# Kernel optimization log

Measured on AMD Instinct MI355X. Metric: run time of the kernel, lower is better.

## Reference

```python
import jax, jax.numpy as jnp
import numpy as np

T, N, E = 6, 50000, 1600000
NFEAT, NHID, NCLASS = 256, 256, 16
SLOPE = 11.0 / 48.0  # eval-mode RReLU: mean of default (lower=1/8, upper=1/3)


def _grcu(H_seq, src, dst, val, Wz, Uz, bz, Wr, Ur, br, Wh, Uh, bh, Q0):
    """One GRCU layer: matrix-GRU weight evolution + sparse GCN aggregation per step.
    H_seq: [T, N, in]  src/dst: [T, E] int  val: [T, E]  Q0: [in, out]."""
    n = H_seq.shape[1]

    def step(Q, xs):
        H, s, d, v = xs
        # mat_GRU_cell: x = hidden = prev_Q (z_topk path is unused in this repo's forward)
        z = jax.nn.sigmoid(Wz @ Q + Uz @ Q + bz)
        r = jax.nn.sigmoid(Wr @ Q + Ur @ Q + br)
        h = jnp.tanh(Wh @ Q + Uh @ (r * Q) + bh)
        Qn = (1.0 - z) * Q + z * h
        XW = H @ Qn                                   # [N, out]
        msg = v[:, None] * XW[s]                      # per-edge gather: Ahat row weights
        agg = jax.ops.segment_sum(msg, d, num_segments=n)  # Ahat @ (H @ Qn)
        out = jnp.where(agg >= 0, agg, SLOPE * agg)   # RReLU (eval)
        return Qn, out

    _, out_seq = jax.lax.scan(step, Q0, (H_seq, src, dst, val))
    return out_seq  # [T, N, out]


def setup_inputs() -> dict:
    key = jax.random.key(0)
    ks = iter(jax.random.split(key, 64))

    def rn(shape, scale=0.05):
        return jax.random.normal(next(ks), shape, dtype=jnp.float32) * scale

    inp = {
        "node_feats": jax.random.normal(next(ks), (T, N, NFEAT), dtype=jnp.float32),
        "edge_val": jax.random.uniform(next(ks), (T, E), dtype=jnp.float32),
    }
    for l, (fi, fo) in enumerate([(NFEAT, NHID), (NHID, NHID)]):
        for g in ("z", "r", "h"):
            inp[f"l{l}_W{g}"] = rn((fi, fi))
            inp[f"l{l}_U{g}"] = rn((fi, fi))
            inp[f"l{l}_b{g}"] = jnp.zeros((fi, fo), dtype=jnp.float32)
        inp[f"l{l}_Q0"] = rn((fi, fo))
    inp["mlp_W1"] = rn((NHID, NHID))
    inp["mlp_b1"] = jnp.zeros((NHID,), dtype=jnp.float32)
    inp["mlp_W2"] = rn((NHID, NCLASS))
    inp["mlp_b2"] = jnp.zeros((NCLASS,), dtype=jnp.float32)
    inp["edge_src"] = jax.random.randint(next(ks), (T, E), 0, N, dtype=jnp.int32)
    inp["edge_dst"] = jax.random.randint(next(ks), (T, E), 0, N, dtype=jnp.int32)
    return inp


def reference(node_feats, edge_val,
              l0_Wz, l0_Uz, l0_bz, l0_Wr, l0_Ur, l0_br, l0_Wh, l0_Uh, l0_bh, l0_Q0,
              l1_Wz, l1_Uz, l1_bz, l1_Wr, l1_Ur, l1_br, l1_Wh, l1_Uh, l1_bh, l1_Q0,
              mlp_W1, mlp_b1, mlp_W2, mlp_b2,
              edge_src, edge_dst):
    h1 = _grcu(node_feats, edge_src, edge_dst, edge_val,
               l0_Wz, l0_Uz, l0_bz, l0_Wr, l0_Ur, l0_br, l0_Wh, l0_Uh, l0_bh, l0_Q0)
    h2 = _grcu(h1, edge_src, edge_dst, edge_val,
               l1_Wz, l1_Uz, l1_bz, l1_Wr, l1_Ur, l1_br, l1_Wh, l1_Uh, l1_bh, l1_Q0)
    out = h2[-1]                                    # last timestep, [N, nhid]
    hid = jax.nn.relu(out @ mlp_W1 + mlp_b1)
    logits = hid @ mlp_W2 + mlp_b2
    return jax.nn.log_softmax(logits, axis=1)       # [N, nclass]
```

## Files before the change

### kernel.cpp

```cpp
#include <hip/hip_runtime.h>
#include <cstddef>

#define SLOPE_F (11.0f / 48.0f)

static const int NN = 50000;
static const int EE = 1600000;
static const int D  = 256;

typedef __attribute__((ext_vector_type(8))) short short8;
typedef __attribute__((ext_vector_type(4))) float f32x4;

__device__ __forceinline__ ushort f2bf(float f) {
    unsigned u = __float_as_uint(f);
    unsigned r = (u + 0x7fffu + ((u >> 16) & 1u)) >> 16;
    return (ushort)r;
}
__device__ __forceinline__ float bf2f(ushort u) {
    return __uint_as_float(((unsigned)u) << 16);
}

__global__ __launch_bounds__(256) void prep_kernel(
        const float* __restrict__ Wz0, const float* __restrict__ Uz0,
        const float* __restrict__ Wr0, const float* __restrict__ Ur0,
        const float* __restrict__ Wh0, const float* __restrict__ Uh0,
        const float* __restrict__ Wz1, const float* __restrict__ Uz1,
        const float* __restrict__ Wr1, const float* __restrict__ Ur1,
        const float* __restrict__ Wh1, const float* __restrict__ Uh1,
        const float* __restrict__ W1,
        float* __restrict__ TW, ushort* __restrict__ BtW1, int* __restrict__ deg) {
    int b = blockIdx.x;
    int t = threadIdx.x;
    if (b < 2048) {
        int mat = b >> 8;
        int k = b & 255;
        const float* P = nullptr; const float* S = nullptr;
        switch (mat) {
            case 0: P = Wz0; S = Uz0; break;
            case 1: P = Wr0; S = Ur0; break;
            case 2: P = Wh0; break;
            case 3: P = Uh0; break;
            case 4: P = Wz1; S = Uz1; break;
            case 5: P = Wr1; S = Ur1; break;
            case 6: P = Wh1; break;
            default: P = Uh1; break;
        }
        float v = P[t * 256 + k];
        if (S) v += S[t * 256 + k];
        TW[((size_t)mat * 256 + k) * 256 + t] = v;
    } else if (b < 2304) {
        int n = b - 2048;
        BtW1[(size_t)n * 256 + t] = f2bf(W1[t * 256 + n]);
    } else {
        int i = (b - 2304) * 256 + t;
        if (i < NN) deg[i] = 0;
    }
}

__global__ __launch_bounds__(256) void gruhist_kernel(
        const float* __restrict__ TW,
        const float* __restrict__ bz0, const float* __restrict__ br0,
        const float* __restrict__ bh0, const float* __restrict__ Q00,
        const float* __restrict__ bz1, const float* __restrict__ br1,
        const float* __restrict__ bh1, const float* __restrict__ Q01,
        ushort* __restrict__ Bt,
        const int* __restrict__ dst, int* __restrict__ deg) {
    if (blockIdx.x >= 256) {
        int e = (blockIdx.x - 256) * 256 + threadIdx.x;
        if (e < EE) atomicAdd(&deg[dst[e]], 1);
        return;
    }
    __shared__ float qs[256][2];
    __shared__ float rqs[256][2];
    int layer = blockIdx.x >> 7;
    int j0 = (blockIdx.x & 127) * 2;
    int i = threadIdx.x;
    const float* MzT = TW + (size_t)layer * 4 * 65536;
    const float* MrT = MzT + 65536;
    const float* WhT = MzT + 2 * 65536;
    const float* UhT = MzT + 3 * 65536;
    const float* bz = layer ? bz1 : bz0;
    const float* br = layer ? br1 : br0;
    const float* bh = layer ? bh1 : bh0;
    const float* Q0 = layer ? Q01 : Q00;

    float2 bzv = *(const float2*)&bz[i * 256 + j0];
    float2 brv = *(const float2*)&br[i * 256 + j0];
    float2 bhv = *(const float2*)&bh[i * 256 + j0];
    float bza[2] = {bzv.x, bzv.y};
    float bra[2] = {brv.x, brv.y};
    float bha[2] = {bhv.x, bhv.y};

    float2 qv = *(const float2*)&Q0[i * 256 + j0];
    *(float2*)&qs[i][0] = qv;
    __syncthreads();

    float qn[2] = {qv.x, qv.y};
    for (int step = 0; step < 6; ++step) {
        float az[2] = {}, ar[2] = {}, ah[2] = {};
#pragma unroll 8
        for (int k = 0; k < 256; ++k) {
            float mz = MzT[k * 256 + i];
            float mr = MrT[k * 256 + i];
            float wh = WhT[k * 256 + i];
            float2 qk = *(const float2*)&qs[k][0];
            float qa[2] = {qk.x, qk.y};
#pragma unroll
            for (int c = 0; c < 2; ++c) {
                az[c] += mz * qa[c];
                ar[c] += mr * qa[c];
                ah[c] += wh * qa[c];
            }
        }
        float z[2], qo[2];
        float2 qown = *(const float2*)&qs[i][0];
        qo[0] = qown.x; qo[1] = qown.y;
        float rq[2];
#pragma unroll
        for (int c = 0; c < 2; ++c) {
            z[c] = 1.f / (1.f + expf(-(az[c] + bza[c])));
            float r = 1.f / (1.f + expf(-(ar[c] + bra[c])));
            rq[c] = r * qo[c];
        }
        float2 rqv; rqv.x = rq[0]; rqv.y = rq[1];
        *(float2*)&rqs[i][0] = rqv;
        __syncthreads();
        float bu[2] = {};
#pragma unroll 8
        for (int k = 0; k < 256; ++k) {
            float uh = UhT[k * 256 + i];
            float2 rk = *(const float2*)&rqs[k][0];
#pragma unroll
            for (int c = 0; c < 2; ++c) bu[c] += uh * ((c == 0) ? rk.x : rk.y);
        }
        float2 qnv;
#pragma unroll
        for (int c = 0; c < 2; ++c) {
            float h = tanhf(ah[c] + bu[c] + bha[c]);
            qn[c] = (1.f - z[c]) * qo[c] + z[c] * h;
        }
        qnv.x = qn[0]; qnv.y = qn[1];
        *(float2*)&qs[i][0] = qnv;
        __syncthreads();
    }
#pragma unroll
    for (int c = 0; c < 2; ++c)
        Bt[(size_t)layer * 65536 + (size_t)(j0 + c) * 256 + i] = f2bf(qn[c]);
}

template <int ASRC, int EPI>
__global__ __launch_bounds__(256) void gemm_mfma(const ushort* __restrict__ A,
                                                 const float* __restrict__ Af,
                                                 const ushort* __restrict__ Bt,
                                                 const float* __restrict__ bias,
                                                 ushort* __restrict__ C, int M) {
    int tid = threadIdx.x;
    int w = tid >> 6, l = tid & 63;
    int lr = l & 15;
    int lk = l >> 4;
    int row0 = blockIdx.x * 128 + w * 32;
    int ra = row0 + lr;      if (ra > M - 1) ra = M - 1;
    int rb = row0 + 16 + lr; if (rb > M - 1) rb = M - 1;
    const ushort* Ap0  = A  + (size_t)ra * 256 + lk * 8;
    const ushort* Ap1  = A  + (size_t)rb * 256 + lk * 8;
    const float*  Apf0 = Af + (size_t)ra * 256 + lk * 8;
    const float*  Apf1 = Af + (size_t)rb * 256 + lk * 8;
    const ushort* Bp   = Bt + (size_t)lr * 256 + lk * 8;

    f32x4 acc0[16] = {};
    f32x4 acc1[16] = {};
#pragma unroll
    for (int kc = 0; kc < 8; ++kc) {
        short8 a0, a1;
        if (ASRC == 0) {
            a0 = *(const short8*)(Ap0 + kc * 32);
            a1 = *(const short8*)(Ap1 + kc * 32);
        } else {
            float4 f0 = *(const float4*)(Apf0 + kc * 32);
            float4 f1 = *(const float4*)(Apf0 + kc * 32 + 4);
            float4 g0 = *(const float4*)(Apf1 + kc * 32);
            float4 g1 = *(const float4*)(Apf1 + kc * 32 + 4);
            a0[0] = (short)f2bf(f0.x); a0[1] = (short)f2bf(f0.y);
            a0[2] = (short)f2bf(f0.z); a0[3] = (short)f2bf(f0.w);
            a0[4] = (short)f2bf(f1.x); a0[5] = (short)f2bf(f1.y);
            a0[6] = (short)f2bf(f1.z); a0[7] = (short)f2bf(f1.w);
            a1[0] = (short)f2bf(g0.x); a1[1] = (short)f2bf(g0.y);
            a1[2] = (short)f2bf(g0.z); a1[3] = (short)f2bf(g0.w);
            a1[4] = (short)f2bf(g1.x); a1[5] = (short)f2bf(g1.y);
            a1[6] = (short)f2bf(g1.z); a1[7] = (short)f2bf(g1.w);
        }
#pragma unroll
        for (int nb = 0; nb < 16; ++nb) {
            short8 bf = *(const short8*)(Bp + (size_t)nb * 4096 + kc * 32);
            acc0[nb] = __builtin_amdgcn_mfma_f32_16x16x32_bf16(a0, bf, acc0[nb], 0, 0, 0);
            acc1[nb] = __builtin_amdgcn_mfma_f32_16x16x32_bf16(a1, bf, acc1[nb], 0, 0, 0);
        }
    }

    int ro = lk * 4;
#pragma unroll
    for (int nb = 0; nb < 16; ++nb) {
        int gc = nb * 16 + lr;
        float bb = (EPI == 1) ? bias[gc] : 0.f;
#pragma unroll
        for (int q = 0; q < 4; ++q) {
            int g0 = row0 + ro + q;
            if (g0 < M) {
                float v = acc0[nb][q];
                if (EPI == 1) v = fmaxf(v + bb, 0.f);
                C[(size_t)g0 * 256 + gc] = f2bf(v);
            }
            int g1 = row0 + 16 + ro + q;
            if (g1 < M) {
                float v = acc1[nb][q];
                if (EPI == 1) v = fmaxf(v + bb, 0.f);
                C[(size_t)g1 * 256 + gc] = f2bf(v);
            }
        }
    }
}

__global__ __launch_bounds__(256) void scanA_kernel(const int* __restrict__ deg,
                                                    int* __restrict__ rs,
                                                    int* __restrict__ bsum, int n) {
    __shared__ int wsum[4];
    int tid = threadIdx.x;
    int i = blockIdx.x * 256 + tid;
    int lane = tid & 63, wv = tid >> 6;
    int v = (i < n) ? deg[i] : 0;
    int x = v;
#pragma unroll
    for (int off = 1; off < 64; off <<= 1) {
        int t = __shfl_up(x, off, 64);
        if (lane >= off) x += t;
    }
    if (lane == 63) wsum[wv] = x;
    __syncthreads();
    if (tid == 0) {
        int s = 0;
#pragma unroll
        for (int q = 0; q < 4; ++q) { int t = wsum[q]; wsum[q] = s; s += t; }
        bsum[blockIdx.x] = s;
    }
    __syncthreads();
    if (i < n) rs[i] = wsum[wv] + x - v;
}

__global__ __launch_bounds__(256) void scanB_kernel(const int* __restrict__ bsum,
                                                    int* __restrict__ boff,
                                                    int* __restrict__ rs, int nb) {
    __shared__ int wsum[4];
    int tid = threadIdx.x;
    int lane = tid & 63, wv = tid >> 6;
    int v = (tid < nb) ? bsum[tid] : 0;
    int x = v;
#pragma unroll
    for (int off = 1; off < 64; off <<= 1) {
        int t = __shfl_up(x, off, 64);
        if (lane >= off) x += t;
    }
    if (lane == 63) wsum[wv] = x;
    __syncthreads();
    if (tid == 0) {
        int s = 0;
#pragma unroll
        for (int q = 0; q < 4; ++q) { int t = wsum[q]; wsum[q] = s; s += t; }
        rs[NN] = EE;
    }
    __syncthreads();
    if (tid < nb) boff[tid] = wsum[wv] + x - v;
}

__global__ __launch_bounds__(256) void scanC_kernel(int* __restrict__ rs,
                                                    int* __restrict__ cur,
                                                    const int* __restrict__ boff, int n) {
    int i = blockIdx.x * 256 + threadIdx.x;
    if (i < n) {
        int v = rs[i] + boff[blockIdx.x];
        rs[i] = v;
        cur[i] = v;
    }
}

__global__ void scatter_kernel(const int* __restrict__ src, const int* __restrict__ dst,
                               const float* __restrict__ val, int* __restrict__ cur,
                               unsigned long long* __restrict__ csr, int nE) {
    int e = blockIdx.x * blockDim.x + threadIdx.x;
    if (e < nE) {
        int p = atomicAdd(&cur[dst[e]], 1);
        unsigned long long pk = (unsigned long long)(unsigned)src[e]
                              | ((unsigned long long)(unsigned)__float_as_uint(val[e]) << 32);
        __builtin_nontemporal_store(pk, &csr[p]);
    }
}

__global__ __launch_bounds__(256) void agg_csr_kernel(const ushort* __restrict__ XW,
                                                      const int2* __restrict__ csr,
                                                      const int* __restrict__ rs,
                                                      ushort* __restrict__ out) {
    int d = blockIdx.x * 4 + (threadIdx.x >> 6);
    if (d >= NN) return;
    int l = threadIdx.x & 63;
    int h = l >> 5;
    int il = l & 31;
    int beg = rs[d], end = rs[d + 1];
    float a0 = 0.f, a1 = 0.f, a2 = 0.f, a3 = 0.f;
    float a4 = 0.f, a5 = 0.f, a6 = 0.f, a7 = 0.f;
    int i = beg + h;
    for (; i + 14 < end; i += 16) {
        int2 e[8];
        short8 x[8];
#pragma unroll
        for (int u = 0; u < 8; ++u) e[u] = csr[i + 2 * u];
#pragma unroll
        for (int u = 0; u < 8; ++u)
            x[u] = *(const short8*)&XW[(size_t)e[u].x * D + il * 8];
#pragma unroll
        for (int u = 0; u < 8; ++u) {
            float v = __int_as_float(e[u].y);
            a0 += v * bf2f((ushort)x[u][0]);
            a1 += v * bf2f((ushort)x[u][1]);
            a2 += v * bf2f((ushort)x[u][2]);
            a3 += v * bf2f((ushort)x[u][3]);
            a4 += v * bf2f((ushort)x[u][4]);
            a5 += v * bf2f((ushort)x[u][5]);
            a6 += v * bf2f((ushort)x[u][6]);
            a7 += v * bf2f((ushort)x[u][7]);
        }
    }
    for (; i + 6 < end; i += 8) {
        int2 e[4];
        short8 x[4];
#pragma unroll
        for (int u = 0; u < 4; ++u) e[u] = csr[i + 2 * u];
#pragma unroll
        for (int u = 0; u < 4; ++u)
            x[u] = *(const short8*)&XW[(size_t)e[u].x * D + il * 8];
#pragma unroll
        for (int u = 0; u < 4; ++u) {
            float v = __int_as_float(e[u].y);
            a0 += v * bf2f((ushort)x[u][0]);
            a1 += v * bf2f((ushort)x[u][1]);
            a2 += v * bf2f((ushort)x[u][2]);
            a3 += v * bf2f((ushort)x[u][3]);
            a4 += v * bf2f((ushort)x[u][4]);
            a5 += v * bf2f((ushort)x[u][5]);
            a6 += v * bf2f((ushort)x[u][6]);
            a7 += v * bf2f((ushort)x[u][7]);
        }
    }
    for (; i < end; i += 2) {
        int2 e0 = csr[i];
        float v0 = __int_as_float(e0.y);
        short8 x0 = *(const short8*)&XW[(size_t)e0.x * D + il * 8];
        a0 += v0 * bf2f((ushort)x0[0]); a1 += v0 * bf2f((ushort)x0[1]);
        a2 += v0 * bf2f((ushort)x0[2]); a3 += v0 * bf2f((ushort)x0[3]);
        a4 += v0 * bf2f((ushort)x0[4]); a5 += v0 * bf2f((ushort)x0[5]);
        a6 += v0 * bf2f((ushort)x0[6]); a7 += v0 * bf2f((ushort)x0[7]);
    }
    a0 += __shfl_xor(a0, 32); a1 += __shfl_xor(a1, 32);
    a2 += __shfl_xor(a2, 32); a3 += __shfl_xor(a3, 32);
    a4 += __shfl_xor(a4, 32); a5 += __shfl_xor(a5, 32);
    a6 += __shfl_xor(a6, 32); a7 += __shfl_xor(a7, 32);
    if (h == 0) {
        float r[8] = {a0, a1, a2, a3, a4, a5, a6, a7};
        short8 o;
#pragma unroll
        for (int c = 0; c < 8; ++c) {
            float v = r[c];
            v = (v >= 0.f) ? v : SLOPE_F * v;
            o[c] = (short)f2bf(v);
        }
        *(short8*)&out[(size_t)d * D + il * 8] = o;
    }
}

__global__ void mlp2_kernel(const ushort* __restrict__ hid, const float* __restrict__ W2,
                            const float* __restrict__ b2, float* __restrict__ out, int M) {
    int tid = threadIdx.x;
    int n = blockIdx.x * 16 + (tid >> 4);
    int c = tid & 15;
    if (n >= M) return;
    float acc = b2[c];
    const ushort* hp = hid + (size_t)n * D;
    for (int k = 0; k < D; k += 8) {
        short8 h8 = *(const short8*)(hp + k);
#pragma unroll
        for (int u = 0; u < 8; ++u)
            acc += bf2f((ushort)h8[u]) * W2[(k + u) * 16 + c];
    }
    float m = acc;
#pragma unroll
    for (int off = 1; off < 16; off <<= 1)
        m = fmaxf(m, __shfl_xor(m, off, 16));
    float ex = expf(acc - m);
    float s = ex;
#pragma unroll
    for (int off = 1; off < 16; off <<= 1)
        s += __shfl_xor(s, off, 16);
    out[(size_t)n * 16 + c] = acc - m - logf(s);
}

extern "C" void kernel_launch(void* const* d_in, const int* in_sizes, int n_in,
                              void* d_out, int out_size, void* d_ws, size_t ws_size,
                              hipStream_t stream) {
    const float* node_feats = (const float*)d_in[0];
    const float* edge_val   = (const float*)d_in[1];
    const float* l0_Wz = (const float*)d_in[2];
    const float* l0_Uz = (const float*)d_in[3];
    const float* l0_bz = (const float*)d_in[4];
    const float* l0_Wr = (const float*)d_in[5];
    const float* l0_Ur = (const float*)d_in[6];
    const float* l0_br = (const float*)d_in[7];
    const float* l0_Wh = (const float*)d_in[8];
    const float* l0_Uh = (const float*)d_in[9];
    const float* l0_bh = (const float*)d_in[10];
    const float* l0_Q0 = (const float*)d_in[11];
    const float* l1_Wz = (const float*)d_in[12];
    const float* l1_Uz = (const float*)d_in[13];
    const float* l1_bz = (const float*)d_in[14];
    const float* l1_Wr = (const float*)d_in[15];
    const float* l1_Ur = (const float*)d_in[16];
    const float* l1_br = (const float*)d_in[17];
    const float* l1_Wh = (const float*)d_in[18];
    const float* l1_Uh = (const float*)d_in[19];
    const float* l1_bh = (const float*)d_in[20];
    const float* l1_Q0 = (const float*)d_in[21];
    const float* W1 = (const float*)d_in[22];
    const float* b1 = (const float*)d_in[23];
    const float* W2 = (const float*)d_in[24];
    const float* b2 = (const float*)d_in[25];
    const int* e_src = (const int*)d_in[26];
    const int* e_dst = (const int*)d_in[27];
    float* out = (float*)d_out;

    const size_t BIG = (size_t)NN * D;
    ushort* XWb = (ushort*)d_ws;
    ushort* H   = XWb + BIG;
    ushort* Bt  = H + BIG;
    float*  TW  = (float*)(Bt + 3 * 65536);
    int2*   csr = (int2*)(TW + 8 * 65536);
    int*    deg = (int*)(csr + EE);
    int*    rs  = deg + NN;
    int*    cur = rs + NN + 1;
    int*    bsum = cur + NN;
    int*    boff = bsum + 200;

    const float* feats5 = node_feats + (size_t)5 * BIG;
    const int*   src5   = e_src + (size_t)5 * EE;
    const int*   dst5   = e_dst + (size_t)5 * EE;
    const float* val5   = edge_val + (size_t)5 * EE;

    prep_kernel<<<2500, 256, 0, stream>>>(l0_Wz, l0_Uz, l0_Wr, l0_Ur, l0_Wh, l0_Uh,
                                          l1_Wz, l1_Uz, l1_Wr, l1_Ur, l1_Wh, l1_Uh,
                                          W1, TW, Bt + 2 * 65536, deg);

    const int histblocks = (EE + 255) / 256;
    gruhist_kernel<<<256 + histblocks, 256, 0, stream>>>(TW, l0_bz, l0_br, l0_bh, l0_Q0,
                                                         l1_bz, l1_br, l1_bh, l1_Q0, Bt,
                                                         dst5, deg);

    const int nchunks = (NN + 255) / 256;
    scanA_kernel<<<nchunks, 256, 0, stream>>>(deg, rs, bsum, NN);
    scanB_kernel<<<1, 256, 0, stream>>>(bsum, boff, rs, nchunks);
    scanC_kernel<<<nchunks, 256, 0, stream>>>(rs, cur, boff, NN);
    scatter_kernel<<<(EE + 255) / 256, 256, 0, stream>>>(src5, dst5, val5, cur,
                                                         (unsigned long long*)csr, EE);

    const int gemm_blocks = (NN + 127) / 128;
    const int ablocks = (NN + 3) / 4;

    gemm_mfma<1, 0><<<gemm_blocks, 256, 0, stream>>>(nullptr, feats5, Bt + 0 * 65536,
                                                     nullptr, XWb, NN);
    agg_csr_kernel<<<ablocks, 256, 0, stream>>>(XWb, csr, rs, H);

    gemm_mfma<0, 0><<<gemm_blocks, 256, 0, stream>>>(H, nullptr, Bt + 1 * 65536,
                                                     nullptr, XWb, NN);
    agg_csr_kernel<<<ablocks, 256, 0, stream>>>(XWb, csr, rs, H);

    gemm_mfma<0, 1><<<gemm_blocks, 256, 0, stream>>>(H, nullptr, Bt + 2 * 65536,
                                                     b1, XWb, NN);
    mlp2_kernel<<<(NN + 15) / 16, 256, 0, stream>>>(XWb, W2, b2, out, NN);
}
```

Before: 685.9 us.

## Merge preprocessing, scan and scatter stages into fewer fused kernel launches

```diff
diff --git a/kernel.cpp b/kernel.cpp
--- a/kernel.cpp
+++ b/kernel.cpp
@@ -6,6 +6,8 @@
 static const int NN = 50000;
 static const int EE = 1600000;
 static const int D  = 256;
+static const int NCH = 196;
+static const int GB  = 391;
 
 typedef __attribute__((ext_vector_type(8))) short short8;
 typedef __attribute__((ext_vector_type(4))) float f32x4;
@@ -19,7 +21,7 @@
     return __uint_as_float(((unsigned)u) << 16);
 }
 
-__global__ __launch_bounds__(256) void prep_kernel(
+__global__ __launch_bounds__(256) void prephist_kernel(
         const float* __restrict__ Wz0, const float* __restrict__ Uz0,
         const float* __restrict__ Wr0, const float* __restrict__ Ur0,
         const float* __restrict__ Wh0, const float* __restrict__ Uh0,
@@ -27,12 +29,19 @@
         const float* __restrict__ Wr1, const float* __restrict__ Ur1,
         const float* __restrict__ Wh1, const float* __restrict__ Uh1,
         const float* __restrict__ W1,
-        float* __restrict__ TW, ushort* __restrict__ BtW1, int* __restrict__ deg) {
+        float* __restrict__ TW, ushort* __restrict__ BtW1,
+        const int* __restrict__ dst, int* __restrict__ deg) {
     int b = blockIdx.x;
-    int t = threadIdx.x;
-    if (b < 2048) {
-        int mat = b >> 8;
-        int k = b & 255;
+    int tid = threadIdx.x;
+    if (b >= 144) {
+        int e = (b - 144) * 256 + tid;
+        if (e < EE) atomicAdd(&deg[dst[e]], 1);
+        return;
+    }
+    __shared__ float lt[64][65];
+    if (b < 128) {
+        int mat = b >> 4;
+        int tr = (b >> 2) & 3, tc = b & 3;
         const float* P = nullptr; const float* S = nullptr;
         switch (mat) {
             case 0: P = Wz0; S = Uz0; break;
@@ -44,36 +53,104 @@
             case 6: P = Wh1; break;
             default: P = Uh1; break;
         }
-        float v = P[t * 256 + k];
-        if (S) v += S[t * 256 + k];
-        TW[((size_t)mat * 256 + k) * 256 + t] = v;
-    } else if (b < 2304) {
-        int n = b - 2048;
-        BtW1[(size_t)n * 256 + t] = f2bf(W1[t * 256 + n]);
+#pragma unroll
+        for (int r0 = 0; r0 < 64; r0 += 4) {
+            int r = r0 + (tid >> 6);
+            int c = tid & 63;
+            int row = tr * 64 + r, col = tc * 64 + c;
+            float v = P[row * 256 + col];
+            if (S) v += S[row * 256 + col];
+            lt[r][c] = v;
+        }
+        __syncthreads();
+#pragma unroll
+        for (int c0 = 0; c0 < 64; c0 += 4) {
+            int c = c0 + (tid >> 6);
+            int r = tid & 63;
+            int row = tr * 64 + r, col = tc * 64 + c;
+            TW[((size_t)mat * 256 + col) * 256 + row] = lt[r][c];
+        }
     } else {
-        int i = (b - 2304) * 256 + t;
-        if (i < NN) deg[i] = 0;
-    }
-}
-
-__global__ __launch_bounds__(256) void gruhist_kernel(
+        int t = b - 128;
+        int tr = (t >> 2) & 3, tc = t & 3;
+#pragma unroll
+        for (int r0 = 0; r0 < 64; r0 += 4) {
+            int r = r0 + (tid >> 6);
+            int c = tid & 63;
+            lt[r][c] = W1[(tr * 64 + r) * 256 + tc * 64 + c];
+        }
+        __syncthreads();
+#pragma unroll
+        for (int c0 = 0; c0 < 64; c0 += 4) {
+            int c = c0 + (tid >> 6);
+            int r = tid & 63;
+            BtW1[(size_t)(tc * 64 + c) * 256 + tr * 64 + r] = f2bf(lt[r][c]);
+        }
+    }
+}
+
+__global__ __launch_bounds__(256) void gruscan_kernel(
         const float* __restrict__ TW,
         const float* __restrict__ bz0, const float* __restrict__ br0,
         const float* __restrict__ bh0, const float* __restrict__ Q00,
         const float* __restrict__ bz1, const float* __restrict__ br1,
         const float* __restrict__ bh1, const float* __restrict__ Q01,
         ushort* __restrict__ Bt,
-        const int* __restrict__ dst, int* __restrict__ deg) {
-    if (blockIdx.x >= 256) {
-        int e = (blockIdx.x - 256) * 256 + threadIdx.x;
-        if (e < EE) atomicAdd(&deg[dst[e]], 1);
+        const int* __restrict__ deg, int* __restrict__ rs, int* __restrict__ cur,
+        int* __restrict__ bsum, int* __restrict__ boff, int* __restrict__ done) {
+    int tid = threadIdx.x;
+    if (blockIdx.x >= 128) {
+        __shared__ int wsum[4];
+        __shared__ int lastflag;
+        int blk = blockIdx.x - 128;
+        int i = blk * 256 + tid;
+        int lane = tid & 63, wv = tid >> 6;
+        int v = (i < NN) ? deg[i] : 0;
+        int x = v;
+#pragma unroll
+        for (int off = 1; off < 64; off <<= 1) {
+            int t = __shfl_up(x, off, 64);
+            if (lane >= off) x += t;
+        }
+        if (lane == 63) wsum[wv] = x;
+        __syncthreads();
+        if (tid == 0) {
+            int s = 0;
+#pragma unroll
+            for (int q = 0; q < 4; ++q) { int t = wsum[q]; wsum[q] = s; s += t; }
+            bsum[blk] = s;
+        }
+        __syncthreads();
+        if (i < NN) { int p = wsum[wv] + x - v; rs[i] = p; cur[i] = p; }
+        __threadfence();
+        if (tid == 0) lastflag = (atomicAdd(done, 1) == NCH - 1);
+        __syncthreads();
+        if (lastflag) {
+            __threadfence();
+            int bv = (tid < NCH) ? bsum[tid] : 0;
+            int bx = bv;
+#pragma unroll
+            for (int off = 1; off < 64; off <<= 1) {
+                int t = __shfl_up(bx, off, 64);
+                if (lane >= off) bx += t;
+            }
+            if (lane == 63) wsum[wv] = bx;
+            __syncthreads();
+            if (tid == 0) {
+                int s = 0;
+#pragma unroll
+                for (int q = 0; q < 4; ++q) { int t = wsum[q]; wsum[q] = s; s += t; }
+            }
+            __syncthreads();
+            if (tid < NCH) boff[tid] = wsum[wv] + bx - bv;
+        }
         return;
     }
-    __shared__ float qs[256][2];
-    __shared__ float rqs[256][2];
-    int layer = blockIdx.x >> 7;
-    int j0 = (blockIdx.x & 127) * 2;
-    int i = threadIdx.x;
+    __shared__ float qs[256][4];
+    __shared__ float rqs[256][4];
+    int layer = blockIdx.x >> 6;
+    int j0 = (blockIdx.x & 63) * 4;
+    int i = tid;
     const float* MzT = TW + (size_t)layer * 4 * 65536;
     const float* MrT = MzT + 65536;
     const float* WhT = MzT + 2 * 65536;
@@ -83,81 +160,82 @@
     const float* bh = layer ? bh1 : bh0;
     const float* Q0 = layer ? Q01 : Q00;
 
-    float2 bzv = *(const float2*)&bz[i * 256 + j0];
-    float2 brv = *(const float2*)&br[i * 256 + j0];
-    float2 bhv = *(const float2*)&bh[i * 256 + j0];
-    float bza[2] = {bzv.x, bzv.y};
-    float bra[2] = {brv.x, brv.y};
-    float bha[2] = {bhv.x, bhv.y};
-
-    float2 qv = *(const float2*)&Q0[i * 256 + j0];
-    *(float2*)&qs[i][0] = qv;
+    float4 bzv = *(const float4*)&bz[i * 256 + j0];
+    float4 brv = *(const float4*)&br[i * 256 + j0];
+    float4 bhv = *(const float4*)&bh[i * 256 + j0];
+    float bza[4] = {bzv.x, bzv.y, bzv.z, bzv.w};
+    float bra[4] = {brv.x, brv.y, brv.z, brv.w};
+    float bha[4] = {bhv.x, bhv.y, bhv.z, bhv.w};
+
+    float4 qv = *(const float4*)&Q0[i * 256 + j0];
+    *(float4*)&qs[i][0] = qv;
     __syncthreads();
 
-    float qn[2] = {qv.x, qv.y};
+    float qn[4] = {qv.x, qv.y, qv.z, qv.w};
     for (int step = 0; step < 6; ++step) {
-        float az[2] = {}, ar[2] = {}, ah[2] = {};
-#pragma unroll 8
+        float az[4] = {}, ar[4] = {}, ah[4] = {};
+#pragma unroll 4
         for (int k = 0; k < 256; ++k) {
             float mz = MzT[k * 256 + i];
             float mr = MrT[k * 256 + i];
             float wh = WhT[k * 256 + i];
-            float2 qk = *(const float2*)&qs[k][0];
-            float qa[2] = {qk.x, qk.y};
-#pragma unroll
-            for (int c = 0; c < 2; ++c) {
+            float4 qk = *(const float4*)&qs[k][0];
+            float qa[4] = {qk.x, qk.y, qk.z, qk.w};
+#pragma unroll
+            for (int c = 0; c < 4; ++c) {
                 az[c] += mz * qa[c];
                 ar[c] += mr * qa[c];
                 ah[c] += wh * qa[c];
             }
         }
-        float z[2], qo[2];
-        float2 qown = *(const float2*)&qs[i][0];
-        qo[0] = qown.x; qo[1] = qown.y;
-        float rq[2];
-#pragma unroll
-        for (int c = 0; c < 2; ++c) {
+        float z[4], qo[4];
+        float4 qown = *(const float4*)&qs[i][0];
+        qo[0] = qown.x; qo[1] = qown.y; qo[2] = qown.z; qo[3] = qown.w;
+        float rq[4];
+#pragma unroll
+        for (int c = 0; c < 4; ++c) {
             z[c] = 1.f / (1.f + expf(-(az[c] + bza[c])));
             float r = 1.f / (1.f + expf(-(ar[c] + bra[c])));
             rq[c] = r * qo[c];
         }
-        float2 rqv; rqv.x = rq[0]; rqv.y = rq[1];
-        *(float2*)&rqs[i][0] = rqv;
-        __syncthreads();
-        float bu[2] = {};
-#pragma unroll 8
+        float4 rqv; rqv.x = rq[0]; rqv.y = rq[1]; rqv.z = rq[2]; rqv.w = rq[3];
+        *(float4*)&rqs[i][0] = rqv;
+        __syncthreads();
+        float bu[4] = {};
+#pragma unroll 4
         for (int k = 0; k < 256; ++k) {
             float uh = UhT[k * 256 + i];
-            float2 rk = *(const float2*)&rqs[k][0];
-#pragma unroll
-            for (int c = 0; c < 2; ++c) bu[c] += uh * ((c == 0) ? rk.x : rk.y);
-        }
-        float2 qnv;
-#pragma unroll
-        for (int c = 0; c < 2; ++c) {
+            float4 rk = *(const float4*)&rqs[k][0];
+            float ra[4] = {rk.x, rk.y, rk.z, rk.w};
+#pragma unroll
+            for (int c = 0; c < 4; ++c) bu[c] += uh * ra[c];
+        }
+        float4 qnv;
+#pragma unroll
+        for (int c = 0; c < 4; ++c) {
             float h = tanhf(ah[c] + bu[c] + bha[c]);
             qn[c] = (1.f - z[c]) * qo[c] + z[c] * h;
         }
-        qnv.x = qn[0]; qnv.y = qn[1];
-        *(float2*)&qs[i][0] = qnv;
-        __syncthreads();
-    }
-#pragma unroll
-    for (int c = 0; c < 2; ++c)
+        qnv.x = qn[0]; qnv.y = qn[1]; qnv.z = qn[2]; qnv.w = qn[3];
+        *(float4*)&qs[i][0] = qnv;
+        __syncthreads();
+    }
+#pragma unroll
+    for (int c = 0; c < 4; ++c)
         Bt[(size_t)layer * 65536 + (size_t)(j0 + c) * 256 + i] = f2bf(qn[c]);
 }
 
 template <int ASRC, int EPI>
-__global__ __launch_bounds__(256) void gemm_mfma(const ushort* __restrict__ A,
-                                                 const float* __restrict__ Af,
-                                                 const ushort* __restrict__ Bt,
-                                                 const float* __restrict__ bias,
-                                                 ushort* __restrict__ C, int M) {
-    int tid = threadIdx.x;
+__device__ __forceinline__ void gemm_body(int bid, int tid,
+                                          const ushort* __restrict__ A,
+                                          const float* __restrict__ Af,
+                                          const ushort* __restrict__ Bt,
+                                          const float* __restrict__ bias,
+                                          ushort* __restrict__ C, int M) {
     int w = tid >> 6, l = tid & 63;
     int lr = l & 15;
     int lk = l >> 4;
-    int row0 = blockIdx.x * 128 + w * 32;
+    int row0 = bid * 128 + w * 32;
     int ra = row0 + lr;      if (ra > M - 1) ra = M - 1;
     int rb = row0 + 16 + lr; if (rb > M - 1) rb = M - 1;
     const ushort* Ap0  = A  + (size_t)ra * 256 + lk * 8;
@@ -219,74 +297,32 @@
     }
 }
 
-__global__ __launch_bounds__(256) void scanA_kernel(const int* __restrict__ deg,
-                                                    int* __restrict__ rs,
-                                                    int* __restrict__ bsum, int n) {
-    __shared__ int wsum[4];
-    int tid = threadIdx.x;
-    int i = blockIdx.x * 256 + tid;
-    int lane = tid & 63, wv = tid >> 6;
-    int v = (i < n) ? deg[i] : 0;
-    int x = v;
-#pragma unroll
-    for (int off = 1; off < 64; off <<= 1) {
-        int t = __shfl_up(x, off, 64);
-        if (lane >= off) x += t;
-    }
-    if (lane == 63) wsum[wv] = x;
-    __syncthreads();
-    if (tid == 0) {
-        int s = 0;
-#pragma unroll
-        for (int q = 0; q < 4; ++q) { int t = wsum[q]; wsum[q] = s; s += t; }
-        bsum[blockIdx.x] = s;
-    }
-    __syncthreads();
-    if (i < n) rs[i] = wsum[wv] + x - v;
-}
-
-__global__ __launch_bounds__(256) void scanB_kernel(const int* __restrict__ bsum,
-                                                    int* __restrict__ boff,
-                                                    int* __restrict__ rs, int nb) {
-    __shared__ int wsum[4];
-    int tid = threadIdx.x;
-    int lane = tid & 63, wv = tid >> 6;
-    int v = (tid < nb) ? bsum[tid] : 0;
-    int x = v;
-#pragma unroll
-    for (int off = 1; off < 64; off <<= 1) {
-        int t = __shfl_up(x, off, 64);
-        if (lane >= off) x += t;
-    }
-    if (lane == 63) wsum[wv] = x;
-    __syncthreads();
-    if (tid == 0) {
-        int s = 0;
-#pragma unroll
-        for (int q = 0; q < 4; ++q) { int t = wsum[q]; wsum[q] = s; s += t; }
-        rs[NN] = EE;
-    }
-    __syncthreads();
-    if (tid < nb) boff[tid] = wsum[wv] + x - v;
-}
-
-__global__ __launch_bounds__(256) void scanC_kernel(int* __restrict__ rs,
-                                                    int* __restrict__ cur,
-                                                    const int* __restrict__ boff, int n) {
-    int i = blockIdx.x * 256 + threadIdx.x;
-    if (i < n) {
-        int v = rs[i] + boff[blockIdx.x];
-        rs[i] = v;
-        cur[i] = v;
-    }
-}
-
-__global__ void scatter_kernel(const int* __restrict__ src, const int* __restrict__ dst,
-                               const float* __restrict__ val, int* __restrict__ cur,
-                               unsigned long long* __restrict__ csr, int nE) {
-    int e = blockIdx.x * blockDim.x + threadIdx.x;
-    if (e < nE) {
-        int p = atomicAdd(&cur[dst[e]], 1);
+template <int ASRC, int EPI>
+__global__ __launch_bounds__(256) void gemm_mfma(const ushort* __restrict__ A,
+                                                 const float* __restrict__ Af,
+                                                 const ushort* __restrict__ Bt,
+                                                 const float* __restrict__ bias,
+                                                 ushort* __restrict__ C, int M) {
+    gemm_body<ASRC, EPI>(blockIdx.x, threadIdx.x, A, Af, Bt, bias, C, M);
+}
+
+__global__ __launch_bounds__(256) void gemsca_kernel(const float* __restrict__ Af,
+                                                     const ushort* __restrict__ Bt,
+                                                     ushort* __restrict__ C, int M,
+                                                     const int* __restrict__ src,
+                                                     const int* __restrict__ dst,
+                                                     const float* __restrict__ val,
+                                                     int* __restrict__ cur,
+                                                     const int* __restrict__ boff,
+                                                     unsigned long long* __restrict__ csr) {
+    if (blockIdx.x < GB) {
+        gemm_body<1, 0>(blockIdx.x, threadIdx.x, nullptr, Af, Bt, nullptr, C, M);
+        return;
+    }
+    int e = (blockIdx.x - GB) * 256 + threadIdx.x;
+    if (e < EE) {
+        int d = dst[e];
+        int p = atomicAdd(&cur[d], 1) + boff[d >> 8];
         unsigned long long pk = (unsigned long long)(unsigned)src[e]
                               | ((unsigned long long)(unsigned)__float_as_uint(val[e]) << 32);
         __builtin_nontemporal_store(pk, &csr[p]);
@@ -296,13 +332,15 @@
 __global__ __launch_bounds__(256) void agg_csr_kernel(const ushort* __restrict__ XW,
                                                       const int2* __restrict__ csr,
                                                       const int* __restrict__ rs,
+                                                      const int* __restrict__ boff,
                                                       ushort* __restrict__ out) {
     int d = blockIdx.x * 4 + (threadIdx.x >> 6);
     if (d >= NN) return;
     int l = threadIdx.x & 63;
     int h = l >> 5;
     int il = l & 31;
-    int beg = rs[d], end = rs[d + 1];
+    int beg = rs[d] + boff[d >> 8];
+    int end = (d + 1 < NN) ? (rs[d + 1] + boff[(d + 1) >> 8]) : EE;
     float a0 = 0.f, a1 = 0.f, a2 = 0.f, a3 = 0.f;
     float a4 = 0.f, a5 = 0.f, a6 = 0.f, a7 = 0.f;
     int i = beg + h;
@@ -440,8 +478,9 @@
     float*  TW  = (float*)(Bt + 3 * 65536);
     int2*   csr = (int2*)(TW + 8 * 65536);
     int*    deg = (int*)(csr + EE);
-    int*    rs  = deg + NN;
-    int*    cur = rs + NN + 1;
+    int*    done = deg + NN;
+    int*    rs  = done + 1;
+    int*    cur = rs + NN;
     int*    bsum = cur + NN;
     int*    boff = bsum + 200;
 
@@ -450,34 +489,29 @@
     const int*   dst5   = e_dst + (size_t)5 * EE;
     const float* val5   = edge_val + (size_t)5 * EE;
 
-    prep_kernel<<<2500, 256, 0, stream>>>(l0_Wz, l0_Uz, l0_Wr, l0_Ur, l0_Wh, l0_Uh,
-                                          l1_Wz, l1_Uz, l1_Wr, l1_Ur, l1_Wh, l1_Uh,
-                                          W1, TW, Bt + 2 * 65536, deg);
+    hipMemsetAsync(deg, 0, (NN + 1) * sizeof(int), stream);
 
     const int histblocks = (EE + 255) / 256;
-    gruhist_kernel<<<256 + histblocks, 256, 0, stream>>>(TW, l0_bz, l0_br, l0_bh, l0_Q0,
-                                                         l1_bz, l1_br, l1_bh, l1_Q0, Bt,
-                                                         dst5, deg);
-
-    const int nchunks = (NN + 255) / 256;
-    scanA_kernel<<<nchunks, 256, 0, stream>>>(deg, rs, bsum, NN);
-    scanB_kernel<<<1, 256, 0, stream>>>(bsum, boff, rs, nchunks);
-    scanC_kernel<<<nchunks, 256, 0, stream>>>(rs, cur, boff, NN);
-    scatter_kernel<<<(EE + 255) / 256, 256, 0, stream>>>(src5, dst5, val5, cur,
-                                                         (unsigned long long*)csr, EE);
-
-    const int gemm_blocks = (NN + 127) / 128;
+    prephist_kernel<<<144 + histblocks, 256, 0, stream>>>(
+        l0_Wz, l0_Uz, l0_Wr, l0_Ur, l0_Wh, l0_Uh,
+        l1_Wz, l1_Uz, l1_Wr, l1_Ur, l1_Wh, l1_Uh,
+        W1, TW, Bt + 2 * 65536, dst5, deg);
+
+    gruscan_kernel<<<128 + NCH, 256, 0, stream>>>(TW, l0_bz, l0_br, l0_bh, l0_Q0,
+                                                  l1_bz, l1_br, l1_bh, l1_Q0, Bt,
+                                                  deg, rs, cur, bsum, boff, done);
+
+    gemsca_kernel<<<GB + histblocks, 256, 0, stream>>>(feats5, Bt + 0 * 65536, XWb, NN,
+                                                       src5, dst5, val5, cur, boff,
+                                                       (unsigned long long*)csr);
+
     const int ablocks = (NN + 3) / 4;
 
-    gemm_mfma<1, 0><<<gemm_blocks, 256, 0, stream>>>(nullptr, feats5, Bt + 0 * 65536,
-                                                     nullptr, XWb, NN);
-    agg_csr_kernel<<<ablocks, 256, 0, stream>>>(XWb, csr, rs, H);
-
-    gemm_mfma<0, 0><<<gemm_blocks, 256, 0, stream>>>(H, nullptr, Bt + 1 * 65536,
-                                                     nullptr, XWb, NN);
-    agg_csr_kernel<<<ablocks, 256, 0, stream>>>(XWb, csr, rs, H);
-
-    gemm_mfma<0, 1><<<gemm_blocks, 256, 0, stream>>>(H, nullptr, Bt + 2 * 65536,
-                                                     b1, XWb, NN);
+    agg_csr_kernel<<<ablocks, 256, 0, stream>>>(XWb, csr, rs, boff, H);
+
+    gemm_mfma<0, 0><<<GB, 256, 0, stream>>>(H, nullptr, Bt + 1 * 65536, nullptr, XWb, NN);
+    agg_csr_kernel<<<ablocks, 256, 0, stream>>>(XWb, csr, rs, boff, H);
+
+    gemm_mfma<0, 1><<<GB, 256, 0, stream>>>(H, nullptr, Bt + 2 * 65536, b1, XWb, NN);
     mlp2_kernel<<<(NN + 15) / 16, 256, 0, stream>>>(XWb, W2, b2, out, NN);
 }
```

After: 714.3 us. 4.1% more time.
